# Kernel optimization log

Measured on AMD Instinct MI355X. Metric: run time of the kernel, lower is better.

## Reference

```python
import jax, jax.numpy as jnp
import numpy as np

BATCH = 4096
NUM_FEATURES = 2048
DEPTH = 4
KERNEL = 2
THRESHOLD = 0.0


def setup_inputs() -> dict:
    key = jax.random.key(0)
    keys = jax.random.split(key, 2 + 2 * DEPTH + 2)
    inp = {}
    inp['x'] = jax.random.normal(keys[0], (BATCH, NUM_FEATURES), dtype=jnp.float32)
    # Conv2d(1,1,kernel_size=2) weight (k,k) and scalar bias, PyTorch-style init scale
    fan_in = KERNEL * KERNEL
    bound = 1.0 / np.sqrt(fan_in)
    inp['conv_w'] = jax.random.uniform(keys[1], (KERNEL, KERNEL), jnp.float32, -bound, bound)
    inp['conv_b'] = jax.random.uniform(keys[2], (), jnp.float32, -bound, bound)
    # MLP hidden layers
    lb = 1.0 / np.sqrt(NUM_FEATURES)
    for i in range(DEPTH):
        inp[f'W{i}'] = jax.random.uniform(keys[3 + 2 * i], (NUM_FEATURES, NUM_FEATURES), jnp.float32, -lb, lb)
        inp[f'b{i}'] = jax.random.uniform(keys[4 + 2 * i], (NUM_FEATURES,), jnp.float32, -lb, lb)
    inp['Wh'] = jax.random.uniform(keys[3 + 2 * DEPTH], (2, NUM_FEATURES), jnp.float32, -lb, lb)
    inp['bh'] = jax.random.uniform(keys[4 + 2 * DEPTH], (2,), jnp.float32, -lb, lb)
    return inp


def reference(x, conv_w, conv_b, W0, b0, W1, b1, W2, b2, W3, b3, Wh, bh):
    # Per-feature ConvFilter on a constant k x k patch of value x_i collapses to
    # sigmoid(x_i * sum(conv_w) + conv_b - threshold)  -- one fused elementwise op.
    h = jax.nn.sigmoid(x * jnp.sum(conv_w) + conv_b - THRESHOLD)  # (B, F)
    for W, b in ((W0, b0), (W1, b1), (W2, b2), (W3, b3)):
        h = jax.nn.relu(h @ W.T + b)
    return h @ Wh.T + bh  # (B, 2)
```

## Files before the change

### kernel.cpp

```cpp
#include <hip/hip_runtime.h>
#include <math.h>

#define BATCH 4096
#define NF    2048

typedef signed char    i8;
typedef unsigned int   u32;
typedef __attribute__((ext_vector_type(4))) int   intx4;
typedef __attribute__((ext_vector_type(4))) float floatx4;

#define LBW 0.022097086912079612f
#define QMAX 32512.0f
#define AMAX_H 3.0f

__global__ __launch_bounds__(256) void prep_kernel(
    const float* __restrict__ x, const float* __restrict__ cw,
    const float* __restrict__ cb,
    const float* __restrict__ w0, const float* __restrict__ w1,
    const float* __restrict__ w2, const float* __restrict__ w3,
    i8* __restrict__ h1o, i8* __restrict__ h2o,
    i8* __restrict__ q1,  i8* __restrict__ q2)
{
    const int bid = blockIdx.x;
    if (bid < 8192) {
        const float s = cw[0] + cw[1] + cw[2] + cw[3];
        const float c = cb[0];
        const int i = bid * 256 + threadIdx.x;
        float4 v = ((const float4*)x)[i];
        float vv[4] = {v.x, v.y, v.z, v.w};
        char4 c1, c2;
        #pragma unroll
        for (int j = 0; j < 4; ++j) {
            float r = 1.0f / (1.0f + expf(-(vv[j] * s + c)));
            int X = (int)(r * QMAX + 0.5f);
            int h1 = (X + 128) >> 8;
            int h2 = X - (h1 << 8);
            ((i8*)&c1)[j] = (i8)h1;
            ((i8*)&c2)[j] = (i8)h2;
        }
        *(char4*)&h1o[(size_t)i * 4] = c1;
        *(char4*)&h2o[(size_t)i * 4] = c2;
    } else {
        const int b2    = bid - 8192;
        const int layer = b2 >> 12;
        const int i     = (b2 & 4095) * 256 + threadIdx.x;
        const float* w = (layer == 0) ? w0 : (layer == 1) ? w1
                       : (layer == 2) ? w2 : w3;
        const size_t base = (size_t)layer * (size_t)NF * NF;
        float4 v = ((const float4*)w)[i];
        float vv[4] = {v.x, v.y, v.z, v.w};
        char4 c1, c2;
        #pragma unroll
        for (int j = 0; j < 4; ++j) {
            int X = (int)floorf(vv[j] * (QMAX / LBW) + 0.5f);
            X = max(-32512, min(32512, X));
            int h1 = (X + 128) >> 8;
            int h2 = X - (h1 << 8);
            ((i8*)&c1)[j] = (i8)h1;
            ((i8*)&c2)[j] = (i8)h2;
        }
        *(char4*)&q1[base + (size_t)i * 4] = c1;
        *(char4*)&q2[base + (size_t)i * 4] = c2;
    }
}

#define BM 256
#define BN 128
#define BK 64

#define BUFSZ  49152
#define SEC_A1 0
#define SEC_A2 16384
#define SEC_B1 32768
#define SEC_B2 40960

__device__ __forceinline__ void stage16(const void* g, void* l) {
    __builtin_amdgcn_global_load_lds(
        (const __attribute__((address_space(1))) u32*)g,
        (__attribute__((address_space(3))) u32*)l, 16, 0, 0);
}

__global__ __launch_bounds__(512, 2) void gemm_i8_split(
    const i8* __restrict__ A1, const i8* __restrict__ A2,
    const i8* __restrict__ B1, const i8* __restrict__ B2,
    const float* __restrict__ bias,
    i8* __restrict__ C1, i8* __restrict__ C2,
    const float* __restrict__ Wh, const float* __restrict__ bh,
    float* __restrict__ outp,
    float combo, float outscale, int last, int M, int N, int K)
{
    extern __shared__ i8 smem[];

    const int t    = threadIdx.x;
    const int wv   = t >> 6;
    const int ln   = t & 63;
    const int quad = ln >> 4;
    const int ml   = ln & 15;
    const int wm   = wv >> 1;
    const int wn   = wv & 1;
    const int bm   = blockIdx.y * BM;
    const int bn   = blockIdx.x * BN;
    const int lnoff = ln * 16;

    int rA0 = (bm + (wv * 2 + 0) * 16 + ml) * K + quad * 16;
    int rA1 = (bm + (wv * 2 + 1) * 16 + ml) * K + quad * 16;
    int rB  = (bn +  wv * 16          + ml) * K + quad * 16;

    intx4 zero = {0, 0, 0, 0};
    intx4 acc11[4][4], accX[4][4];
    #pragma unroll
    for (int i = 0; i < 4; ++i)
        #pragma unroll
        for (int j = 0; j < 4; ++j) { acc11[i][j] = zero; accX[i][j] = zero; }

    stage16(A1 + rA0, smem + 0 * BUFSZ + SEC_A1 + (wv * 2 + 0) * 1024);
    stage16(A1 + rA1, smem + 0 * BUFSZ + SEC_A1 + (wv * 2 + 1) * 1024);
    stage16(A2 + rA0, smem + 0 * BUFSZ + SEC_A2 + (wv * 2 + 0) * 1024);
    stage16(A2 + rA1, smem + 0 * BUFSZ + SEC_A2 + (wv * 2 + 1) * 1024);
    stage16(B1 + rB,  smem + 0 * BUFSZ + SEC_B1 + wv * 1024);
    stage16(B2 + rB,  smem + 0 * BUFSZ + SEC_B2 + wv * 1024);
    rA0 += BK; rA1 += BK; rB += BK;
    stage16(A1 + rA0, smem + 1 * BUFSZ + SEC_A1 + (wv * 2 + 0) * 1024);
    stage16(A1 + rA1, smem + 1 * BUFSZ + SEC_A1 + (wv * 2 + 1) * 1024);
    stage16(A2 + rA0, smem + 1 * BUFSZ + SEC_A2 + (wv * 2 + 0) * 1024);
    stage16(A2 + rA1, smem + 1 * BUFSZ + SEC_A2 + (wv * 2 + 1) * 1024);
    stage16(B1 + rB,  smem + 1 * BUFSZ + SEC_B1 + wv * 1024);
    stage16(B2 + rB,  smem + 1 * BUFSZ + SEC_B2 + wv * 1024);
    rA0 += BK; rA1 += BK; rB += BK;
    asm volatile("s_waitcnt vmcnt(6)" ::: "memory");
    __builtin_amdgcn_s_barrier();
    asm volatile("" ::: "memory");

    int rdbase = 0;
    int wrbase = 2 * BUFSZ;

#define LDA_(SEC, c) (*(const intx4*)&smem[rdbase + (SEC) + (c) * 1024 + lnoff])

    const int NIT = K >> 6;
    #pragma unroll 1
    for (int kt = 0; kt < NIT; ++kt) {
        const int sg = (kt < NIT - 2);
        if (sg) {
            stage16(A1 + rA0, smem + wrbase + SEC_A1 + (wv * 2 + 0) * 1024);
            stage16(A1 + rA1, smem + wrbase + SEC_A1 + (wv * 2 + 1) * 1024);
            stage16(A2 + rA0, smem + wrbase + SEC_A2 + (wv * 2 + 0) * 1024);
            stage16(A2 + rA1, smem + wrbase + SEC_A2 + (wv * 2 + 1) * 1024);
            stage16(B1 + rB,  smem + wrbase + SEC_B1 + wv * 1024);
            stage16(B2 + rB,  smem + wrbase + SEC_B2 + wv * 1024);
            rA0 += BK; rA1 += BK; rB += BK;
        }
        intx4 a1[4], a2[4], b1[4], b2[4];
        #pragma unroll
        for (int i = 0; i < 4; ++i) {
            a1[i] = LDA_(SEC_A1, wm * 4 + i);
            a2[i] = LDA_(SEC_A2, wm * 4 + i);
            b1[i] = LDA_(SEC_B1, wn * 4 + i);
            b2[i] = LDA_(SEC_B2, wn * 4 + i);
        }
        #pragma unroll
        for (int j = 0; j < 4; ++j) {
            #pragma unroll
            for (int i = 0; i < 4; ++i) {
                acc11[i][j] = __builtin_amdgcn_mfma_i32_16x16x64_i8(a1[i], b1[j], acc11[i][j], 0, 0, 0);
                accX [i][j] = __builtin_amdgcn_mfma_i32_16x16x64_i8(a1[i], b2[j], accX [i][j], 0, 0, 0);
                accX [i][j] = __builtin_amdgcn_mfma_i32_16x16x64_i8(a2[i], b1[j], accX [i][j], 0, 0, 0);
            }
        }
        if (sg) { asm volatile("s_waitcnt vmcnt(6)" ::: "memory"); }
        else    { asm volatile("s_waitcnt vmcnt(0)" ::: "memory"); }
        __builtin_amdgcn_s_barrier();
        asm volatile("" ::: "memory");
        rdbase = (rdbase == 2 * BUFSZ) ? 0 : rdbase + BUFSZ;
        wrbase = (wrbase == 2 * BUFSZ) ? 0 : wrbase + BUFSZ;
    }

#undef LDA_

    if (!last) {
        #pragma unroll
        for (int j = 0; j < 4; ++j) {
            const int n  = bn + wn * 64 + j * 16 + ml;
            const float bv = bias[n];
            #pragma unroll
            for (int i = 0; i < 4; ++i) {
                #pragma unroll
                for (int r = 0; r < 4; ++r) {
                    const int m = bm + wm * 64 + i * 16 + quad * 4 + r;
                    float v = fmaf(65536.0f, (float)acc11[i][j][r],
                                   256.0f * (float)accX[i][j][r]) * combo + bv;
                    v = fmaxf(v, 0.0f);
                    int X = (int)(fminf(v * outscale, QMAX) + 0.5f);
                    int h1 = (X + 128) >> 8;
                    int h2 = X - (h1 << 8);
                    C1[(size_t)m * N + n] = (i8)h1;
                    C2[(size_t)m * N + n] = (i8)h2;
                }
            }
        }
    } else {
        float wh0[4], wh1[4], bv[4];
        #pragma unroll
        for (int j = 0; j < 4; ++j) {
            const int n = bn + wn * 64 + j * 16 + ml;
            bv[j]  = bias[n];
            wh0[j] = Wh[n];
            wh1[j] = Wh[NF + n];
        }
        #pragma unroll
        for (int i = 0; i < 4; ++i) {
            #pragma unroll
            for (int r = 0; r < 4; ++r) {
                float s0 = 0.0f, s1 = 0.0f;
                #pragma unroll
                for (int j = 0; j < 4; ++j) {
                    float v = fmaf(65536.0f, (float)acc11[i][j][r],
                                   256.0f * (float)accX[i][j][r]) * combo + bv[j];
                    v = fmaxf(v, 0.0f);
                    s0 = fmaf(v, wh0[j], s0);
                    s1 = fmaf(v, wh1[j], s1);
                }
                #pragma unroll
                for (int off = 8; off > 0; off >>= 1) {
                    s0 += __shfl_xor(s0, off, 64);
                    s1 += __shfl_xor(s1, off, 64);
                }
                if (ml == 0) {
                    const int m = bm + wm * 64 + i * 16 + quad * 4 + r;
                    if (bn == 0 && wn == 0) { s0 += bh[0]; s1 += bh[1]; }
                    atomicAdd(&outp[(size_t)m * 2 + 0], s0);
                    atomicAdd(&outp[(size_t)m * 2 + 1], s1);
                }
            }
        }
    }
}

__global__ __launch_bounds__(256) void act_kernel_f32(
    const float* __restrict__ x, const float* __restrict__ conv_w,
    const float* __restrict__ conv_b, float* __restrict__ h, int n4)
{
    const float s = conv_w[0] + conv_w[1] + conv_w[2] + conv_w[3];
    const float c = conv_b[0];
    int i = blockIdx.x * blockDim.x + threadIdx.x;
    if (i < n4) {
        float4 v = ((const float4*)x)[i];
        float4 r;
        r.x = 1.0f / (1.0f + expf(-(v.x * s + c)));
        r.y = 1.0f / (1.0f + expf(-(v.y * s + c)));
        r.z = 1.0f / (1.0f + expf(-(v.z * s + c)));
        r.w = 1.0f / (1.0f + expf(-(v.w * s + c)));
        ((float4*)h)[i] = r;
    }
}

#define FBM 128
#define FBN 128
#define FBK 16
#define FPAD 4

__global__ __launch_bounds__(256) void gemm_bias_relu_f32(
    const float* __restrict__ A, const float* __restrict__ W,
    const float* __restrict__ bias, float* __restrict__ C,
    int M, int N, int K, int do_relu)
{
    __shared__ float As[FBK][FBM + FPAD];
    __shared__ float Bs[FBK][FBN + FPAD];
    const int t  = threadIdx.x;
    const int bm = blockIdx.y * FBM;
    const int bn = blockIdx.x * FBN;
    const int tn = (t & 15) * 8;
    const int tm = (t >> 4) * 8;
    const int r0 = t >> 2;
    const int kv = (t & 3) << 2;
    float acc[8][8] = {};
    for (int k0 = 0; k0 < K; k0 += FBK) {
        #pragma unroll
        for (int half = 0; half < 2; ++half) {
            const int row = r0 + half * 64;
            float4 av = *(const float4*)&A[(size_t)(bm + row) * K + k0 + kv];
            As[kv + 0][row] = av.x; As[kv + 1][row] = av.y;
            As[kv + 2][row] = av.z; As[kv + 3][row] = av.w;
            float4 bv = *(const float4*)&W[(size_t)(bn + row) * K + k0 + kv];
            Bs[kv + 0][row] = bv.x; Bs[kv + 1][row] = bv.y;
            Bs[kv + 2][row] = bv.z; Bs[kv + 3][row] = bv.w;
        }
        __syncthreads();
        #pragma unroll
        for (int kk = 0; kk < FBK; ++kk) {
            float a[8], b[8];
            *(float4*)&a[0] = *(const float4*)&As[kk][tm];
            *(float4*)&a[4] = *(const float4*)&As[kk][tm + 4];
            *(float4*)&b[0] = *(const float4*)&Bs[kk][tn];
            *(float4*)&b[4] = *(const float4*)&Bs[kk][tn + 4];
            #pragma unroll
            for (int i = 0; i < 8; ++i)
                #pragma unroll
                for (int j = 0; j < 8; ++j)
                    acc[i][j] = fmaf(a[i], b[j], acc[i][j]);
        }
        __syncthreads();
    }
    #pragma unroll
    for (int i = 0; i < 8; ++i) {
        const int row = bm + tm + i;
        #pragma unroll
        for (int j = 0; j < 8; j += 4) {
            float4 v;
            v.x = acc[i][j + 0] + bias[bn + tn + j + 0];
            v.y = acc[i][j + 1] + bias[bn + tn + j + 1];
            v.z = acc[i][j + 2] + bias[bn + tn + j + 2];
            v.w = acc[i][j + 3] + bias[bn + tn + j + 3];
            if (do_relu) {
                v.x = fmaxf(v.x, 0.0f); v.y = fmaxf(v.y, 0.0f);
                v.z = fmaxf(v.z, 0.0f); v.w = fmaxf(v.w, 0.0f);
            }
            *(float4*)&C[(size_t)row * N + bn + tn + j] = v;
        }
    }
}

__global__ __launch_bounds__(256) void head_kernel_f32(
    const float* __restrict__ h, const float* __restrict__ Wh,
    const float* __restrict__ bh, float* __restrict__ out)
{
    const int wave = threadIdx.x >> 6;
    const int lane = threadIdx.x & 63;
    const int row  = blockIdx.x * 4 + wave;
    const float* hr = h + (size_t)row * NF;
    float acc0 = 0.0f, acc1 = 0.0f;
    for (int k = lane * 4; k < NF; k += 256) {
        float4 v  = *(const float4*)&hr[k];
        float4 w0 = *(const float4*)&Wh[k];
        float4 w1 = *(const float4*)&Wh[NF + k];
        acc0 += v.x * w0.x + v.y * w0.y + v.z * w0.z + v.w * w0.w;
        acc1 += v.x * w1.x + v.y * w1.y + v.z * w1.z + v.w * w1.w;
    }
    #pragma unroll
    for (int off = 32; off > 0; off >>= 1) {
        acc0 += __shfl_down(acc0, off, 64);
        acc1 += __shfl_down(acc1, off, 64);
    }
    if (lane == 0) {
        out[row * 2 + 0] = acc0 + bh[0];
        out[row * 2 + 1] = acc1 + bh[1];
    }
}

extern "C" void kernel_launch(void* const* d_in, const int* in_sizes, int n_in,
                              void* d_out, int out_size, void* d_ws, size_t ws_size,
                              hipStream_t stream)
{
    const float* x      = (const float*)d_in[0];
    const float* conv_w = (const float*)d_in[1];
    const float* conv_b = (const float*)d_in[2];
    const float* Ws[4]  = {(const float*)d_in[3], (const float*)d_in[5],
                           (const float*)d_in[7], (const float*)d_in[9]};
    const float* bs[4]  = {(const float*)d_in[4], (const float*)d_in[6],
                           (const float*)d_in[8], (const float*)d_in[10]};
    const float* Wh     = (const float*)d_in[11];
    const float* bh     = (const float*)d_in[12];
    float* out = (float*)d_out;

    const size_t AE = (size_t)BATCH * NF;
    const size_t WE = (size_t)NF * NF;
    const size_t need_i8 = 4 * AE + 8 * WE;

    const int n4 = (BATCH * NF) / 4;

    if (ws_size >= need_i8) {
        static int attr_done = 0;
        if (!attr_done) {
            (void)hipFuncSetAttribute(
                reinterpret_cast<const void*>(gemm_i8_split),
                hipFuncAttributeMaxDynamicSharedMemorySize, 3 * BUFSZ);
            attr_done = 1;
        }

        i8* base = (i8*)d_ws;
        i8* a01 = base;
        i8* a02 = a01 + AE;
        i8* a11 = a02 + AE;
        i8* a12 = a11 + AE;
        i8* wq1 = a12 + AE;
        i8* wq2 = wq1 + 4 * WE;

        hipMemsetAsync(out, 0, (size_t)out_size * sizeof(float), stream);

        prep_kernel<<<8192 + 16384, 256, 0, stream>>>(
            x, conv_w, conv_b, Ws[0], Ws[1], Ws[2], Ws[3],
            a01, a02, wq1, wq2);

        const float sW = LBW / QMAX;
        const float outscale = QMAX / AMAX_H;
        dim3 grid(NF / BN, BATCH / BM);

        i8 *in1 = a01, *in2 = a02, *o1 = a11, *o2 = a12;
        for (int l = 0; l < 4; ++l) {
            const float sA = ((l == 0) ? 1.0f : AMAX_H) / QMAX;
            gemm_i8_split<<<grid, 512, 3 * BUFSZ, stream>>>(
                in1, in2, wq1 + (size_t)l * WE, wq2 + (size_t)l * WE,
                bs[l], o1, o2, Wh, bh, out,
                sA * sW, outscale, (l == 3) ? 1 : 0, BATCH, NF, NF);
            i8* t1 = in1; i8* t2 = in2;
            in1 = o1; in2 = o2; o1 = t1; o2 = t2;
        }
    } else {
        float* ws0 = (float*)d_ws;
        float* ws1 = ws0 + AE;
        act_kernel_f32<<<(n4 + 255) / 256, 256, 0, stream>>>(x, conv_w, conv_b, ws0, n4);
        dim3 fgrid(NF / FBN, BATCH / FBM);
        gemm_bias_relu_f32<<<fgrid, 256, 0, stream>>>(ws0, Ws[0], bs[0], ws1, BATCH, NF, NF, 1);
        gemm_bias_relu_f32<<<fgrid, 256, 0, stream>>>(ws1, Ws[1], bs[1], ws0, BATCH, NF, NF, 1);
        gemm_bias_relu_f32<<<fgrid, 256, 0, stream>>>(ws0, Ws[2], bs[2], ws1, BATCH, NF, NF, 1);
        gemm_bias_relu_f32<<<fgrid, 256, 0, stream>>>(ws1, Ws[3], bs[3], ws0, BATCH, NF, NF, 1);
        head_kernel_f32<<<BATCH / 4, 256, 0, stream>>>(ws0, Wh, bh, out);
    }
}
```

Measured before the change: 363.8 us.

## Load B operand tiles directly to registers, staging only A through LDS

The B (weight) fragments are now fetched straight from global memory into registers, double-buffered across two register sets with the k-loop unrolled by two. Only the A tiles are staged through LDS via global_load_lds, which shrinks the shared-memory footprint from 3×48KB to 3×32KB and removes the B LDS reads. The cost is more VGPR pressure from the register-held B buffers, B loads repeated by the waves that share a wn column, and hand-tuned vmcnt waits that must match the load counts exactly.

```diff
diff --git a/kernel.cpp b/kernel.cpp
--- a/kernel.cpp
+++ b/kernel.cpp
@@ -68,11 +68,8 @@
 #define BN 128
 #define BK 64
 
-#define BUFSZ  49152
-#define SEC_A1 0
+#define ABUF   32768
 #define SEC_A2 16384
-#define SEC_B1 32768
-#define SEC_B2 40960
 
 __device__ __forceinline__ void stage16(const void* g, void* l) {
     __builtin_amdgcn_global_load_lds(
@@ -104,7 +101,10 @@
 
     int rA0 = (bm + (wv * 2 + 0) * 16 + ml) * K + quad * 16;
     int rA1 = (bm + (wv * 2 + 1) * 16 + ml) * K + quad * 16;
-    int rB  = (bn +  wv * 16          + ml) * K + quad * 16;
+    int rB0 = (bn + (wn * 4 + 0) * 16 + ml) * K + quad * 16;
+    int rB1 = rB0 + 16 * K;
+    int rB2 = rB0 + 32 * K;
+    int rB3 = rB0 + 48 * K;
 
     intx4 zero = {0, 0, 0, 0};
     intx4 acc11[4][4], accX[4][4];
@@ -113,68 +113,98 @@
         #pragma unroll
         for (int j = 0; j < 4; ++j) { acc11[i][j] = zero; accX[i][j] = zero; }
 
-    stage16(A1 + rA0, smem + 0 * BUFSZ + SEC_A1 + (wv * 2 + 0) * 1024);
-    stage16(A1 + rA1, smem + 0 * BUFSZ + SEC_A1 + (wv * 2 + 1) * 1024);
-    stage16(A2 + rA0, smem + 0 * BUFSZ + SEC_A2 + (wv * 2 + 0) * 1024);
-    stage16(A2 + rA1, smem + 0 * BUFSZ + SEC_A2 + (wv * 2 + 1) * 1024);
-    stage16(B1 + rB,  smem + 0 * BUFSZ + SEC_B1 + wv * 1024);
-    stage16(B2 + rB,  smem + 0 * BUFSZ + SEC_B2 + wv * 1024);
-    rA0 += BK; rA1 += BK; rB += BK;
-    stage16(A1 + rA0, smem + 1 * BUFSZ + SEC_A1 + (wv * 2 + 0) * 1024);
-    stage16(A1 + rA1, smem + 1 * BUFSZ + SEC_A1 + (wv * 2 + 1) * 1024);
-    stage16(A2 + rA0, smem + 1 * BUFSZ + SEC_A2 + (wv * 2 + 0) * 1024);
-    stage16(A2 + rA1, smem + 1 * BUFSZ + SEC_A2 + (wv * 2 + 1) * 1024);
-    stage16(B1 + rB,  smem + 1 * BUFSZ + SEC_B1 + wv * 1024);
-    stage16(B2 + rB,  smem + 1 * BUFSZ + SEC_B2 + wv * 1024);
-    rA0 += BK; rA1 += BK; rB += BK;
-    asm volatile("s_waitcnt vmcnt(6)" ::: "memory");
+    intx4 bXa1[4], bXa2[4];
+    intx4 bYa1[4], bYa2[4];
+
+#define FENCE_ asm volatile("" ::: "memory")
+#define LDG_(P, off) (*(const intx4*)&(P)[off])
+#define LDA_(SEC, c) (*(const intx4*)&smem[rdbase + (SEC) + (c) * 1024 + lnoff])
+
+    stage16(A1 + rA0, smem + 0 * ABUF + (wv * 2 + 0) * 1024);
+    stage16(A1 + rA1, smem + 0 * ABUF + (wv * 2 + 1) * 1024);
+    stage16(A2 + rA0, smem + 0 * ABUF + SEC_A2 + (wv * 2 + 0) * 1024);
+    stage16(A2 + rA1, smem + 0 * ABUF + SEC_A2 + (wv * 2 + 1) * 1024);
+    rA0 += BK; rA1 += BK;
+    FENCE_;
+    bXa1[0] = LDG_(B1, rB0); bXa1[1] = LDG_(B1, rB1);
+    bXa1[2] = LDG_(B1, rB2); bXa1[3] = LDG_(B1, rB3);
+    bXa2[0] = LDG_(B2, rB0); bXa2[1] = LDG_(B2, rB1);
+    bXa2[2] = LDG_(B2, rB2); bXa2[3] = LDG_(B2, rB3);
+    rB0 += BK; rB1 += BK; rB2 += BK; rB3 += BK;
+    FENCE_;
+    stage16(A1 + rA0, smem + 1 * ABUF + (wv * 2 + 0) * 1024);
+    stage16(A1 + rA1, smem + 1 * ABUF + (wv * 2 + 1) * 1024);
+    stage16(A2 + rA0, smem + 1 * ABUF + SEC_A2 + (wv * 2 + 0) * 1024);
+    stage16(A2 + rA1, smem + 1 * ABUF + SEC_A2 + (wv * 2 + 1) * 1024);
+    rA0 += BK; rA1 += BK;
+    asm volatile("s_waitcnt vmcnt(12)" ::: "memory");
     __builtin_amdgcn_s_barrier();
-    asm volatile("" ::: "memory");
+    FENCE_;
 
     int rdbase = 0;
-    int wrbase = 2 * BUFSZ;
-
-#define LDA_(SEC, c) (*(const intx4*)&smem[rdbase + (SEC) + (c) * 1024 + lnoff])
+    int wrbase = 2 * ABUF;
 
     const int NIT = K >> 6;
+
+#define KBODY(KT, BC1, BC2, BX1, BX2) { \
+    const int kt_ = (KT); \
+     \
+    if (kt_ < NIT - 1) { \
+        BX1[0] = LDG_(B1, rB0); BX1[1] = LDG_(B1, rB1); \
+        BX1[2] = LDG_(B1, rB2); BX1[3] = LDG_(B1, rB3); \
+        BX2[0] = LDG_(B2, rB0); BX2[1] = LDG_(B2, rB1); \
+        BX2[2] = LDG_(B2, rB2); BX2[3] = LDG_(B2, rB3); \
+        rB0 += BK; rB1 += BK; rB2 += BK; rB3 += BK; \
+    } \
+    FENCE_; \
+     \
+    if (kt_ < NIT - 2) { \
+        stage16(A1 + rA0, smem + wrbase + (wv * 2 + 0) * 1024); \
+        stage16(A1 + rA1, smem + wrbase + (wv * 2 + 1) * 1024); \
+        stage16(A2 + rA0, smem + wrbase + SEC_A2 + (wv * 2 + 0) * 1024); \
+        stage16(A2 + rA1, smem + wrbase + SEC_A2 + (wv * 2 + 1) * 1024); \
+        rA0 += BK; rA1 += BK; \
+    } \
+    FENCE_; \
+     \
+    intx4 a1[4], a2[4]; \
+    _Pragma("unroll") \
+    for (int i = 0; i < 4; ++i) { \
+        a1[i] = LDA_(0,      wm * 4 + i); \
+        a2[i] = LDA_(SEC_A2, wm * 4 + i); \
+    } \
+     \
+    if (kt_ < NIT - 2)       { asm volatile("s_waitcnt vmcnt(16)" ::: "memory"); } \
+    else if (kt_ == NIT - 2) { asm volatile("s_waitcnt vmcnt(12)" ::: "memory"); } \
+    else                     { asm volatile("s_waitcnt vmcnt(0)"  ::: "memory"); } \
+    _Pragma("unroll") \
+    for (int j = 0; j < 4; ++j) { \
+        _Pragma("unroll") \
+        for (int i = 0; i < 4; ++i) { \
+            acc11[i][j] = __builtin_amdgcn_mfma_i32_16x16x64_i8(a1[i], BC1[j], acc11[i][j], 0, 0, 0); \
+            accX [i][j] = __builtin_amdgcn_mfma_i32_16x16x64_i8(a1[i], BC2[j], accX [i][j], 0, 0, 0); \
+            accX [i][j] = __builtin_amdgcn_mfma_i32_16x16x64_i8(a2[i], BC1[j], accX [i][j], 0, 0, 0); \
+        } \
+    } \
+     \
+    if (kt_ < NIT - 2)       { asm volatile("s_waitcnt vmcnt(12)" ::: "memory"); } \
+    else if (kt_ == NIT - 2) { asm volatile("s_waitcnt vmcnt(8)"  ::: "memory"); } \
+    __builtin_amdgcn_s_barrier(); \
+    FENCE_; \
+    rdbase = (rdbase == 2 * ABUF) ? 0 : rdbase + ABUF; \
+    wrbase = (wrbase == 2 * ABUF) ? 0 : wrbase + ABUF; \
+}
+
     #pragma unroll 1
-    for (int kt = 0; kt < NIT; ++kt) {
-        const int sg = (kt < NIT - 2);
-        if (sg) {
-            stage16(A1 + rA0, smem + wrbase + SEC_A1 + (wv * 2 + 0) * 1024);
-            stage16(A1 + rA1, smem + wrbase + SEC_A1 + (wv * 2 + 1) * 1024);
-            stage16(A2 + rA0, smem + wrbase + SEC_A2 + (wv * 2 + 0) * 1024);
-            stage16(A2 + rA1, smem + wrbase + SEC_A2 + (wv * 2 + 1) * 1024);
-            stage16(B1 + rB,  smem + wrbase + SEC_B1 + wv * 1024);
-            stage16(B2 + rB,  smem + wrbase + SEC_B2 + wv * 1024);
-            rA0 += BK; rA1 += BK; rB += BK;
-        }
-        intx4 a1[4], a2[4], b1[4], b2[4];
-        #pragma unroll
-        for (int i = 0; i < 4; ++i) {
-            a1[i] = LDA_(SEC_A1, wm * 4 + i);
-            a2[i] = LDA_(SEC_A2, wm * 4 + i);
-            b1[i] = LDA_(SEC_B1, wn * 4 + i);
-            b2[i] = LDA_(SEC_B2, wn * 4 + i);
-        }
-        #pragma unroll
-        for (int j = 0; j < 4; ++j) {
-            #pragma unroll
-            for (int i = 0; i < 4; ++i) {
-                acc11[i][j] = __builtin_amdgcn_mfma_i32_16x16x64_i8(a1[i], b1[j], acc11[i][j], 0, 0, 0);
-                accX [i][j] = __builtin_amdgcn_mfma_i32_16x16x64_i8(a1[i], b2[j], accX [i][j], 0, 0, 0);
-                accX [i][j] = __builtin_amdgcn_mfma_i32_16x16x64_i8(a2[i], b1[j], accX [i][j], 0, 0, 0);
-            }
-        }
-        if (sg) { asm volatile("s_waitcnt vmcnt(6)" ::: "memory"); }
-        else    { asm volatile("s_waitcnt vmcnt(0)" ::: "memory"); }
-        __builtin_amdgcn_s_barrier();
-        asm volatile("" ::: "memory");
-        rdbase = (rdbase == 2 * BUFSZ) ? 0 : rdbase + BUFSZ;
-        wrbase = (wrbase == 2 * BUFSZ) ? 0 : wrbase + BUFSZ;
-    }
-
+    for (int it = 0; it < NIT / 2; ++it) {
+        KBODY(2 * it,     bXa1, bXa2, bYa1, bYa2)
+        KBODY(2 * it + 1, bYa1, bYa2, bXa1, bXa2)
+    }
+
+#undef KBODY
 #undef LDA_
+#undef LDG_
+#undef FENCE_
 
     if (!last) {
         #pragma unroll
@@ -372,7 +402,7 @@
         if (!attr_done) {
             (void)hipFuncSetAttribute(
                 reinterpret_cast<const void*>(gemm_i8_split),
-                hipFuncAttributeMaxDynamicSharedMemorySize, 3 * BUFSZ);
+                hipFuncAttributeMaxDynamicSharedMemorySize, 3 * ABUF);
             attr_done = 1;
         }
 
@@ -397,7 +427,7 @@
         i8 *in1 = a01, *in2 = a02, *o1 = a11, *o2 = a12;
         for (int l = 0; l < 4; ++l) {
             const float sA = ((l == 0) ? 1.0f : AMAX_H) / QMAX;
-            gemm_i8_split<<<grid, 512, 3 * BUFSZ, stream>>>(
+            gemm_i8_split<<<grid, 512, 3 * ABUF, stream>>>(
                 in1, in2, wq1 + (size_t)l * WE, wq2 + (size_t)l * WE,
                 bs[l], o1, o2, Wh, bh, out,
                 sA * sW, outscale, (l == 3) ? 1 : 0, BATCH, NF, NF);
```

Result: slower. 561.4 us (+54.3%).

## Shrink GEMM tile to 128x128 with 256 threads and double-buffered LDS

Applied to the files above, without the earlier changes.

Halves the M tile and thread count per block, giving twice as many blocks, and moves from a three-stage LDS ring buffer to a two-stage double buffer with a full vmcnt(0) wait each iteration. The smaller LDS footprint (64KB vs 144KB) is meant to let more blocks reside per CU and improve occupancy and load balance. In exchange, prefetch depth drops to one stage so global-load latency is less hidden, and B-tile reuse per block falls.

```diff
diff --git a/kernel.cpp b/kernel.cpp
--- a/kernel.cpp
+++ b/kernel.cpp
@@ -64,15 +64,14 @@
     }
 }
 
-#define BM 256
+#define BM 128
 #define BN 128
 #define BK 64
 
-#define BUFSZ  49152
-#define SEC_A1 0
-#define SEC_A2 16384
-#define SEC_B1 32768
-#define SEC_B2 40960
+#define BUFSZ  32768
+#define SEC_A2 8192
+#define SEC_B1 16384
+#define SEC_B2 24576
 
 __device__ __forceinline__ void stage16(const void* g, void* l) {
     __builtin_amdgcn_global_load_lds(
@@ -80,7 +79,7 @@
         (__attribute__((address_space(3))) u32*)l, 16, 0, 0);
 }
 
-__global__ __launch_bounds__(512, 2) void gemm_i8_split(
+__global__ __launch_bounds__(256, 2) void gemm_i8_split(
     const i8* __restrict__ A1, const i8* __restrict__ A2,
     const i8* __restrict__ B1, const i8* __restrict__ B2,
     const float* __restrict__ bias,
@@ -104,7 +103,8 @@
 
     int rA0 = (bm + (wv * 2 + 0) * 16 + ml) * K + quad * 16;
     int rA1 = (bm + (wv * 2 + 1) * 16 + ml) * K + quad * 16;
-    int rB  = (bn +  wv * 16          + ml) * K + quad * 16;
+    int rB0 = (bn + (wv * 2 + 0) * 16 + ml) * K + quad * 16;
+    int rB1 = (bn + (wv * 2 + 1) * 16 + ml) * K + quad * 16;
 
     intx4 zero = {0, 0, 0, 0};
     intx4 acc11[4][4], accX[4][4];
@@ -113,49 +113,47 @@
         #pragma unroll
         for (int j = 0; j < 4; ++j) { acc11[i][j] = zero; accX[i][j] = zero; }
 
-    stage16(A1 + rA0, smem + 0 * BUFSZ + SEC_A1 + (wv * 2 + 0) * 1024);
-    stage16(A1 + rA1, smem + 0 * BUFSZ + SEC_A1 + (wv * 2 + 1) * 1024);
-    stage16(A2 + rA0, smem + 0 * BUFSZ + SEC_A2 + (wv * 2 + 0) * 1024);
-    stage16(A2 + rA1, smem + 0 * BUFSZ + SEC_A2 + (wv * 2 + 1) * 1024);
-    stage16(B1 + rB,  smem + 0 * BUFSZ + SEC_B1 + wv * 1024);
-    stage16(B2 + rB,  smem + 0 * BUFSZ + SEC_B2 + wv * 1024);
-    rA0 += BK; rA1 += BK; rB += BK;
-    stage16(A1 + rA0, smem + 1 * BUFSZ + SEC_A1 + (wv * 2 + 0) * 1024);
-    stage16(A1 + rA1, smem + 1 * BUFSZ + SEC_A1 + (wv * 2 + 1) * 1024);
-    stage16(A2 + rA0, smem + 1 * BUFSZ + SEC_A2 + (wv * 2 + 0) * 1024);
-    stage16(A2 + rA1, smem + 1 * BUFSZ + SEC_A2 + (wv * 2 + 1) * 1024);
-    stage16(B1 + rB,  smem + 1 * BUFSZ + SEC_B1 + wv * 1024);
-    stage16(B2 + rB,  smem + 1 * BUFSZ + SEC_B2 + wv * 1024);
-    rA0 += BK; rA1 += BK; rB += BK;
-    asm volatile("s_waitcnt vmcnt(6)" ::: "memory");
+#define FENCE_ asm volatile("" ::: "memory")
+#define LDS_(OFF) (*(const intx4*)&smem[(OFF) + lnoff])
+
+    stage16(A1 + rA0, smem + (wv * 2 + 0) * 1024);
+    stage16(A1 + rA1, smem + (wv * 2 + 1) * 1024);
+    stage16(A2 + rA0, smem + SEC_A2 + (wv * 2 + 0) * 1024);
+    stage16(A2 + rA1, smem + SEC_A2 + (wv * 2 + 1) * 1024);
+    stage16(B1 + rB0, smem + SEC_B1 + (wv * 2 + 0) * 1024);
+    stage16(B1 + rB1, smem + SEC_B1 + (wv * 2 + 1) * 1024);
+    stage16(B2 + rB0, smem + SEC_B2 + (wv * 2 + 0) * 1024);
+    stage16(B2 + rB1, smem + SEC_B2 + (wv * 2 + 1) * 1024);
+    rA0 += BK; rA1 += BK; rB0 += BK; rB1 += BK;
+    asm volatile("s_waitcnt vmcnt(0)" ::: "memory");
     __builtin_amdgcn_s_barrier();
-    asm volatile("" ::: "memory");
-
-    int rdbase = 0;
-    int wrbase = 2 * BUFSZ;
-
-#define LDA_(SEC, c) (*(const intx4*)&smem[rdbase + (SEC) + (c) * 1024 + lnoff])
+    FENCE_;
+
+    int rd = 0;
 
     const int NIT = K >> 6;
     #pragma unroll 1
     for (int kt = 0; kt < NIT; ++kt) {
-        const int sg = (kt < NIT - 2);
-        if (sg) {
-            stage16(A1 + rA0, smem + wrbase + SEC_A1 + (wv * 2 + 0) * 1024);
-            stage16(A1 + rA1, smem + wrbase + SEC_A1 + (wv * 2 + 1) * 1024);
-            stage16(A2 + rA0, smem + wrbase + SEC_A2 + (wv * 2 + 0) * 1024);
-            stage16(A2 + rA1, smem + wrbase + SEC_A2 + (wv * 2 + 1) * 1024);
-            stage16(B1 + rB,  smem + wrbase + SEC_B1 + wv * 1024);
-            stage16(B2 + rB,  smem + wrbase + SEC_B2 + wv * 1024);
-            rA0 += BK; rA1 += BK; rB += BK;
-        }
+        const int wr = BUFSZ - rd;
+        if (kt < NIT - 1) {
+            stage16(A1 + rA0, smem + wr + (wv * 2 + 0) * 1024);
+            stage16(A1 + rA1, smem + wr + (wv * 2 + 1) * 1024);
+            stage16(A2 + rA0, smem + wr + SEC_A2 + (wv * 2 + 0) * 1024);
+            stage16(A2 + rA1, smem + wr + SEC_A2 + (wv * 2 + 1) * 1024);
+            stage16(B1 + rB0, smem + wr + SEC_B1 + (wv * 2 + 0) * 1024);
+            stage16(B1 + rB1, smem + wr + SEC_B1 + (wv * 2 + 1) * 1024);
+            stage16(B2 + rB0, smem + wr + SEC_B2 + (wv * 2 + 0) * 1024);
+            stage16(B2 + rB1, smem + wr + SEC_B2 + (wv * 2 + 1) * 1024);
+            rA0 += BK; rA1 += BK; rB0 += BK; rB1 += BK;
+        }
+        FENCE_;
         intx4 a1[4], a2[4], b1[4], b2[4];
         #pragma unroll
         for (int i = 0; i < 4; ++i) {
-            a1[i] = LDA_(SEC_A1, wm * 4 + i);
-            a2[i] = LDA_(SEC_A2, wm * 4 + i);
-            b1[i] = LDA_(SEC_B1, wn * 4 + i);
-            b2[i] = LDA_(SEC_B2, wn * 4 + i);
+            a1[i] = LDS_(rd + (wm * 4 + i) * 1024);
+            a2[i] = LDS_(rd + SEC_A2 + (wm * 4 + i) * 1024);
+            b1[i] = LDS_(rd + SEC_B1 + (wn * 4 + i) * 1024);
+            b2[i] = LDS_(rd + SEC_B2 + (wn * 4 + i) * 1024);
         }
         #pragma unroll
         for (int j = 0; j < 4; ++j) {
@@ -166,15 +164,14 @@
                 accX [i][j] = __builtin_amdgcn_mfma_i32_16x16x64_i8(a2[i], b1[j], accX [i][j], 0, 0, 0);
             }
         }
-        if (sg) { asm volatile("s_waitcnt vmcnt(6)" ::: "memory"); }
-        else    { asm volatile("s_waitcnt vmcnt(0)" ::: "memory"); }
+        asm volatile("s_waitcnt vmcnt(0)" ::: "memory");
         __builtin_amdgcn_s_barrier();
-        asm volatile("" ::: "memory");
-        rdbase = (rdbase == 2 * BUFSZ) ? 0 : rdbase + BUFSZ;
-        wrbase = (wrbase == 2 * BUFSZ) ? 0 : wrbase + BUFSZ;
-    }
-
-#undef LDA_
+        FENCE_;
+        rd = wr;
+    }
+
+#undef LDS_
+#undef FENCE_
 
     if (!last) {
         #pragma unroll
@@ -372,7 +369,7 @@
         if (!attr_done) {
             (void)hipFuncSetAttribute(
                 reinterpret_cast<const void*>(gemm_i8_split),
-                hipFuncAttributeMaxDynamicSharedMemorySize, 3 * BUFSZ);
+                hipFuncAttributeMaxDynamicSharedMemorySize, 2 * BUFSZ);
             attr_done = 1;
         }
 
@@ -397,7 +394,7 @@
         i8 *in1 = a01, *in2 = a02, *o1 = a11, *o2 = a12;
         for (int l = 0; l < 4; ++l) {
             const float sA = ((l == 0) ? 1.0f : AMAX_H) / QMAX;
-            gemm_i8_split<<<grid, 512, 3 * BUFSZ, stream>>>(
+            gemm_i8_split<<<grid, 256, 2 * BUFSZ, stream>>>(
                 in1, in2, wq1 + (size_t)l * WE, wq2 + (size_t)l * WE,
                 bs[l], o1, o2, Wh, bh, out,
                 sA * sW, outscale, (l == 3) ? 1 : 0, BATCH, NF, NF);
```

After: 419.9 us. 1.15x slower.
